# Kernel tuning notes

Hardware: AMD Instinct MI355X
Metric: run time of the kernel (lower is better)

## Reference

```python
import jax, jax.numpy as jnp
import numpy as np
from itertools import combinations

NUM_ENT = 7
DIM_ENT = 256
REL_HIDDEN = 256
HIDDEN = 1024
BATCH = 16384
PAIRS = np.array(list(combinations(range(NUM_ENT), 2)), dtype=np.int32)  # [21, 2]


def setup_inputs() -> dict:
    key = jax.random.key(0)
    k1, k2, k3 = jax.random.split(key, 3)
    ctx = jax.random.normal(k1, (BATCH, NUM_ENT * DIM_ENT), dtype=jnp.float32)
    # torch init: uniform(-init_range, init_range) weights, zero bias
    W_rel = jax.random.uniform(k2, (2 * DIM_ENT, REL_HIDDEN), dtype=jnp.float32, minval=-0.01, maxval=0.01)
    b_rel = jnp.zeros((REL_HIDDEN,), dtype=jnp.float32)
    W_fc = jax.random.uniform(k3, (NUM_ENT * DIM_ENT + REL_HIDDEN, HIDDEN), dtype=jnp.float32, minval=-0.01, maxval=0.01)
    b_fc = jnp.zeros((HIDDEN,), dtype=jnp.float32)
    return {"ctx": ctx, "W_rel": W_rel, "b_rel": b_rel, "W_fc": W_fc, "b_fc": b_fc}


def reference(ctx, W_rel, b_rel, W_fc, b_fc):
    B = ctx.shape[0]
    ents = ctx.reshape(B, NUM_ENT, DIM_ENT)
    idx_i = jnp.asarray(PAIRS[:, 0])
    idx_j = jnp.asarray(PAIRS[:, 1])
    # gather both endpoints of each of the 21 pairs: [B, 21, 2*DIM_ENT]
    pair_feat = jnp.concatenate([ents[:, idx_i, :], ents[:, idx_j, :]], axis=-1)
    # batched small Linear + Tanh: [B, 21, REL_HIDDEN]
    rel = jnp.tanh(jnp.einsum("bpe,eh->bph", pair_feat, W_rel) + b_rel)
    # faithful replication of torch: cat pair-major then view(B, rel_hidden, -1).sum(2)
    rel = rel.reshape(B, 21 * REL_HIDDEN).reshape(B, REL_HIDDEN, 21).sum(axis=2)
    inpt = jnp.concatenate([ctx, rel], axis=1)  # [B, input_size]
    # dropout output is discarded in the original forward (no-op); fc1 uses inpt
    out = jnp.tanh(inpt @ W_fc + b_fc)
    return out[None, :, :]  # [1, B, HIDDEN]
```

## Files before the change

kernel.cpp:

```cpp
#include <hip/hip_runtime.h>

typedef unsigned short u16;
typedef unsigned int u32;
typedef __attribute__((ext_vector_type(8))) short short8;
typedef __attribute__((ext_vector_type(4))) float f32x4;
typedef const __attribute__((address_space(1))) unsigned int g_u32;
typedef __attribute__((address_space(3))) unsigned int l_u32;

#define BATCH 16384
#define XCOLS 2048

__device__ __forceinline__ void gload16(const void* g, void* l) {
  __builtin_amdgcn_global_load_lds((g_u32*)g, (l_u32*)l, 16, 0, 0);
}
__device__ __forceinline__ u16 f2bf(float f) {
  u32 x = __builtin_bit_cast(u32, f);
  x += 0x7fffu + ((x >> 16) & 1u);
  return (u16)(x >> 16);
}
__device__ __forceinline__ int swz(int P) { return P ^ (((P >> 7) & 7) << 4); }

__device__ __forceinline__ float fast_tanh(float x) {
  float e = __builtin_amdgcn_exp2f(x * 2.885390081777927f);
  return __builtin_fmaf(-2.0f, __builtin_amdgcn_rcpf(e + 1.0f), 1.0f);
}

#define PIPK 0544333222211111000000ULL
#define PJPK 0665654654365432654321ULL

__global__ void prep_all(const float* __restrict__ ctx, const float* __restrict__ Wr,
                         const float* __restrict__ Wfc, u16* __restrict__ X,
                         u16* __restrict__ WcT, u16* __restrict__ WfcT) {
  __shared__ float t[64][65];
  const int bid = blockIdx.x, tid = threadIdx.x;
  if (bid < 2048) {
    const int total = BATCH * 224;
    for (int u = bid * 256 + tid; u < total; u += 2048 * 256) {
      int b = u / 224, c8 = u - b * 224;
      const float4* s = (const float4*)(ctx + (size_t)b * 1792 + c8 * 8);
      float4 v0 = s[0], v1 = s[1];
      short8 o;
      o[0] = (short)f2bf(v0.x); o[1] = (short)f2bf(v0.y);
      o[2] = (short)f2bf(v0.z); o[3] = (short)f2bf(v0.w);
      o[4] = (short)f2bf(v1.x); o[5] = (short)f2bf(v1.y);
      o[6] = (short)f2bf(v1.z); o[7] = (short)f2bf(v1.w);
      *(short8*)(X + (size_t)b * XCOLS + c8 * 8) = o;
    }
  } else if (bid < 2560) {
    int b2 = bid - 2048;
    int k0 = (b2 >> 4) * 64, n0 = (b2 & 15) * 64;
    int tx = tid & 63, ty = tid >> 6;
    #pragma unroll
    for (int i = 0; i < 64; i += 4)
      t[ty + i][tx] = Wfc[(size_t)(k0 + ty + i) * 1024 + n0 + tx];
    __syncthreads();
    #pragma unroll
    for (int i = 0; i < 64; i += 4) {
      int n = ty + i;
      WfcT[(size_t)(n0 + n) * XCOLS + k0 + tx] = f2bf(t[tx][n]);
    }
  } else {
    int idx = (bid - 2560) * 256 + tid;
    int n = idx >> 8, k = idx & 255;
    float v = (n < 256) ? Wr[k * 256 + n] : Wr[(256 + k) * 256 + (n - 256)];
    WcT[idx] = f2bf(v);
  }
}

__global__ __launch_bounds__(512, 4) void gemm1_fused(u16* __restrict__ X, const u16* __restrict__ WcT,
                                                      const float* __restrict__ b_rel) {
  __shared__ __align__(16) u16 smem[36864];
  char* sb = (char*)smem;
  const int tid = threadIdx.x;
  const int wid = tid >> 6, lane = tid & 63;
  const int b_base = blockIdx.x * 8;
  f32x4 bias[4] = {};
  if (wid < 4) {
    #pragma unroll
    for (int n = 0; n < 4; ++n)
      bias[n] = *(const f32x4*)(b_rel + wid * 64 + n * 16 + ((lane >> 4) << 2));
  }
  f32x4 acc[4][4] = {};
  for (int kt = 0; kt < 4; ++kt) {
    const int kb = kt * 64;
    {
      int L = swz(tid * 16);
      int row = L >> 7, koff = (L & 127) >> 1;
      int r = row < 56 ? row : 55;
      int bl = r / 7, e = r - bl * 7;
      gload16(X + (size_t)(b_base + bl) * XCOLS + e * 256 + kb + koff, sb + wid * 1024);
    }
    #pragma unroll
    for (int i = 0; i < 8; ++i) {
      int slot = i * 512 + tid;
      int L = swz(slot * 16);
      int rn = L >> 7, koff = (L & 127) >> 1;
      gload16(WcT + rn * 256 + kb + koff, sb + 8192 + (i * 512 + wid * 64) * 16);
    }
    __syncthreads();
    #pragma unroll
    for (int kk = 0; kk < 64; kk += 32) {
      short8 a[4], b[4];
      #pragma unroll
      for (int m = 0; m < 4; ++m) {
        int row = m * 16 + (lane & 15);
        int L = row * 128 + kk * 2 + ((lane >> 4) << 4);
        a[m] = *(const short8*)(sb + swz(L));
      }
      #pragma unroll
      for (int n = 0; n < 4; ++n) {
        int rn = wid * 64 + n * 16 + (lane & 15);
        int L = rn * 128 + kk * 2 + ((lane >> 4) << 4);
        b[n] = *(const short8*)(sb + 8192 + swz(L));
      }
      #pragma unroll
      for (int m = 0; m < 4; ++m)
        #pragma unroll
        for (int n = 0; n < 4; ++n)
          acc[m][n] = __builtin_amdgcn_mfma_f32_16x16x32_bf16(b[n], a[m], acc[m][n], 0, 0, 0);
    }
    __syncthreads();
  }
  float* Tbuf = (float*)(sb + 28672);
  auto stage = [&](int rd) {
    #pragma unroll
    for (int m = 0; m < 4; ++m) {
      int row = m * 16 + (lane & 15);
      int lr = row - rd * 14;
      if (lr >= 0 && lr < 14) {
        #pragma unroll
        for (int n = 0; n < 4; ++n) {
          f32x4 val = acc[m][n] + bias[n];
          int h0 = wid * 64 + n * 16 + ((lane >> 4) << 2);
          int L = lr * 2048 + h0 * 4;
          *(f32x4*)(sb + (L ^ ((lr & 7) << 4))) = val;
        }
      }
    }
  };
  stage(0);
  __syncthreads();
  for (int rd = 0; rd < 4; ++rd) {
    for (int i = tid; i < 2688; i += 512) {
      int bb = i >= 1344;
      int k4 = (i - bb * 1344) << 2;
      int p = k4 >> 8, h0 = k4 & 255;
      int li = bb * 7 + (int)((PIPK >> (3 * p)) & 7);
      int lj = bb * 7 + (int)((PJPK >> (3 * p)) & 7);
      int Lu = (li * 2048 + h0 * 4) ^ ((li & 7) << 4);
      int Lv = (lj * 2048 + 1024 + h0 * 4) ^ ((lj & 7) << 4);
      f32x4 uu = *(const f32x4*)(sb + Lu);
      f32x4 vv = *(const f32x4*)(sb + Lv);
      f32x4 t;
      t[0] = fast_tanh(uu[0] + vv[0]);
      t[1] = fast_tanh(uu[1] + vv[1]);
      t[2] = fast_tanh(uu[2] + vv[2]);
      t[3] = fast_tanh(uu[3] + vv[3]);
      *(f32x4*)(sb + 28672 + (bb * 5376 + k4) * 4) = t;
    }
    __syncthreads();
    {
      int bb = tid >> 8, r = tid & 255;
      const float* T = Tbuf + bb * 5376 + r * 21;
      float s = 0.f;
      #pragma unroll
      for (int c = 0; c < 21; ++c) s += T[c];
      X[(size_t)(b_base + rd * 2 + bb) * XCOLS + 1792 + r] = f2bf(s);
    }
    if (rd < 3) stage(rd + 1);
    __syncthreads();
  }
}

#define G2B 65536
__global__ __launch_bounds__(512, 2) void gemm2(const u16* __restrict__ X, const u16* __restrict__ WT,
                                                const float* __restrict__ b_fc, float* __restrict__ out) {
  __shared__ __align__(16) u16 smem[65536];
  char* sb = (char*)smem;
  const int tid = threadIdx.x;
  const int wid = tid >> 6, lane = tid & 63;
  const int wr = wid >> 2, wc = wid & 3;
  const int bm = blockIdx.x >> 2, bn = blockIdx.x & 3;
  const size_t mBase = (size_t)bm * 256;
  const int nBase = bn * 256;
  f32x4 acc[8][4] = {};
  auto stage2 = [&](int t, int q) {
    char* Ab = sb + q * G2B;
    char* Bb = Ab + 32768;
    const int kb = t * 64;
    #pragma unroll
    for (int i = 0; i < 4; ++i) {
      int L = swz((i * 512 + tid) * 16);
      int row = L >> 7, koff = (L & 127) >> 1;
      int dst = (i * 512 + wid * 64) * 16;
      gload16(X + (mBase + row) * XCOLS + kb + koff, Ab + dst);
      gload16(WT + (size_t)(nBase + row) * XCOLS + kb + koff, Bb + dst);
    }
  };
  auto compute = [&](int q) {
    char* Ab = sb + q * G2B;
    char* Bb = Ab + 32768;
    #pragma unroll
    for (int kk = 0; kk < 64; kk += 32) {
      short8 a[8], b[4];
      #pragma unroll
      for (int m = 0; m < 8; ++m) {
        int row = wr * 128 + m * 16 + (lane & 15);
        int L = row * 128 + kk * 2 + ((lane >> 4) << 4);
        a[m] = *(const short8*)(Ab + swz(L));
      }
      #pragma unroll
      for (int n = 0; n < 4; ++n) {
        int rn = wc * 64 + n * 16 + (lane & 15);
        int L = rn * 128 + kk * 2 + ((lane >> 4) << 4);
        b[n] = *(const short8*)(Bb + swz(L));
      }
      __builtin_amdgcn_s_setprio(1);
      #pragma unroll
      for (int m = 0; m < 8; ++m)
        #pragma unroll
        for (int n = 0; n < 4; ++n)
          acc[m][n] = __builtin_amdgcn_mfma_f32_16x16x32_bf16(a[m], b[n], acc[m][n], 0, 0, 0);
      __builtin_amdgcn_s_setprio(0);
    }
  };
  stage2(0, 0);
  stage2(1, 1);
  for (int t = 0; t < 32; ++t) {
    if (t < 30) asm volatile("s_waitcnt vmcnt(8)" ::: "memory");
    else        asm volatile("s_waitcnt vmcnt(0)" ::: "memory");
    __builtin_amdgcn_s_barrier();
    compute(t & 1);
    if (t < 30) {
      __builtin_amdgcn_s_barrier();
      stage2(t + 2, t & 1);
    }
  }
  #pragma unroll
  for (int m = 0; m < 8; ++m) {
    int row0 = wr * 128 + m * 16 + ((lane >> 4) << 2);
    #pragma unroll
    for (int n = 0; n < 4; ++n) {
      int col = nBase + wc * 64 + n * 16 + (lane & 15);
      float bias = b_fc[col];
      #pragma unroll
      for (int v = 0; v < 4; ++v)
        out[(mBase + row0 + v) * 1024 + col] = fast_tanh(acc[m][n][v] + bias);
    }
  }
}

extern "C" void kernel_launch(void* const* d_in, const int* in_sizes, int n_in,
                              void* d_out, int out_size, void* d_ws, size_t ws_size,
                              hipStream_t stream) {
  const float* ctx   = (const float*)d_in[0];
  const float* W_rel = (const float*)d_in[1];
  const float* b_rel = (const float*)d_in[2];
  const float* W_fc  = (const float*)d_in[3];
  const float* b_fc  = (const float*)d_in[4];
  float* out = (float*)d_out;
  u16* X    = (u16*)d_ws;
  u16* WcT  = X + (size_t)BATCH * XCOLS;
  u16* WfcT = WcT + 512 * 256;
  prep_all<<<3072, 256, 0, stream>>>(ctx, W_rel, W_fc, X, WcT, WfcT);
  gemm1_fused<<<2048, 512, 0, stream>>>(X, WcT, b_rel);
  gemm2<<<256, 512, 0, stream>>>(X, WfcT, b_fc, out);
}
```

Baseline: 192.3 us.

## Fuse pair tanh with row reduction and double-buffer relation staging

The separate pass that wrote tanh values into a temporary LDS buffer is replaced by a per-thread loop. Each thread computes its 21 contiguous flattened tanh entries directly from the staged u/v rows and accumulates them in three partial sums. The u/v staging moves to padded rows (stride 2064) in two alternating buffers. This removes one barrier per round and the temporary buffer traffic, and lets the next stage overlap with the current reduction. The cost is scalar, unvectorized LDS reads with possible bank conflicts, and the accumulation order of the sum changes.

```diff
diff --git a/kernel.cpp b/kernel.cpp
--- a/kernel.cpp
+++ b/kernel.cpp
@@ -9,6 +9,8 @@
 
 #define BATCH 16384
 #define XCOLS 2048
+#define UVROW 2064
+#define UVBUF 28896
 
 __device__ __forceinline__ void gload16(const void* g, void* l) {
   __builtin_amdgcn_global_load_lds((g_u32*)g, (l_u32*)l, 16, 0, 0);
@@ -121,8 +123,8 @@
     }
     __syncthreads();
   }
-  float* Tbuf = (float*)(sb + 28672);
   auto stage = [&](int rd) {
+    char* ub = sb + (rd & 1) * UVBUF;
     #pragma unroll
     for (int m = 0; m < 4; ++m) {
       int row = m * 16 + (lane & 15);
@@ -131,42 +133,41 @@
         #pragma unroll
         for (int n = 0; n < 4; ++n) {
           f32x4 val = acc[m][n] + bias[n];
-          int h0 = wid * 64 + n * 16 + ((lane >> 4) << 2);
-          int L = lr * 2048 + h0 * 4;
-          *(f32x4*)(sb + (L ^ ((lr & 7) << 4))) = val;
+          int h0c = wid * 64 + n * 16 + ((lane >> 4) << 2);
+          *(f32x4*)(ub + lr * UVROW + h0c * 4) = val;
         }
       }
     }
   };
   stage(0);
+  const int bb = tid >> 8;
+  const int r = tid & 255;
+  const int R21 = r * 21;
+  const int p0 = R21 >> 8;
+  const int h0 = R21 & 255;
+  const int cx = 256 - h0;
+  const int p1 = p0 < 20 ? p0 + 1 : 20;
+  const int li0 = bb * 7 + (int)((PIPK >> (3 * p0)) & 7);
+  const int lj0 = bb * 7 + (int)((PJPK >> (3 * p0)) & 7);
+  const int li1 = bb * 7 + (int)((PIPK >> (3 * p1)) & 7);
+  const int lj1 = bb * 7 + (int)((PJPK >> (3 * p1)) & 7);
+  const int bU0 = li0 * UVROW + h0 * 4;
+  const int bV0 = lj0 * UVROW + 1024 + h0 * 4;
+  const int bU1 = li1 * UVROW - cx * 4;
+  const int bV1 = lj1 * UVROW + 1024 - cx * 4;
   __syncthreads();
   for (int rd = 0; rd < 4; ++rd) {
-    for (int i = tid; i < 2688; i += 512) {
-      int bb = i >= 1344;
-      int k4 = (i - bb * 1344) << 2;
-      int p = k4 >> 8, h0 = k4 & 255;
-      int li = bb * 7 + (int)((PIPK >> (3 * p)) & 7);
-      int lj = bb * 7 + (int)((PJPK >> (3 * p)) & 7);
-      int Lu = (li * 2048 + h0 * 4) ^ ((li & 7) << 4);
-      int Lv = (lj * 2048 + 1024 + h0 * 4) ^ ((lj & 7) << 4);
-      f32x4 uu = *(const f32x4*)(sb + Lu);
-      f32x4 vv = *(const f32x4*)(sb + Lv);
-      f32x4 t;
-      t[0] = fast_tanh(uu[0] + vv[0]);
-      t[1] = fast_tanh(uu[1] + vv[1]);
-      t[2] = fast_tanh(uu[2] + vv[2]);
-      t[3] = fast_tanh(uu[3] + vv[3]);
-      *(f32x4*)(sb + 28672 + (bb * 5376 + k4) * 4) = t;
-    }
-    __syncthreads();
-    {
-      int bb = tid >> 8, r = tid & 255;
-      const float* T = Tbuf + bb * 5376 + r * 21;
-      float s = 0.f;
-      #pragma unroll
-      for (int c = 0; c < 21; ++c) s += T[c];
-      X[(size_t)(b_base + rd * 2 + bb) * XCOLS + 1792 + r] = f2bf(s);
-    }
+    const char* ub = sb + (rd & 1) * UVBUF;
+    float s0 = 0.f, s1 = 0.f, s2 = 0.f;
+    #pragma unroll
+    for (int c = 0; c < 21; ++c) {
+      bool sg = c >= cx;
+      float u = *(const float*)(ub + (sg ? bU1 : bU0) + 4 * c);
+      float v = *(const float*)(ub + (sg ? bV1 : bV0) + 4 * c);
+      float t = fast_tanh(u + v);
+      if (c % 3 == 0) s0 += t; else if (c % 3 == 1) s1 += t; else s2 += t;
+    }
+    X[(size_t)(b_base + rd * 2 + bb) * XCOLS + 1792 + r] = f2bf(s0 + s1 + s2);
     if (rd < 3) stage(rd + 1);
     __syncthreads();
   }
```

Result: slower. 234.2 us (+21.8%).
